# Optimization experiments

Hardware: AMD Instinct MI355X
Metric: run time of the kernel (lower is better)

## Reference

```python
import jax, jax.numpy as jnp
import numpy as np

MU = 0.34
STD = 0.04
PATCH = 32
LOG_NORM_CONST = float(np.log(STD * np.sqrt(2.0 * np.pi)))


def _patch_means(unet_output, patch):
    # unet_output: [B, C, H, W] with B == 1 (original code implicitly requires it).
    B, C, H, W = unet_output.shape
    hp, wp = H // patch, W // patch
    x = unet_output.reshape(B * C, hp, patch, wp, patch)
    # mean over batch*channel and both intra-patch axes -> [hp, wp]
    return x.mean(axis=(0, 2, 4))


def reference(unet_output, transformer_output):
    means = _patch_means(unet_output, PATCH)              # [hp, wp]
    mask = transformer_output[0] >= 0.5                   # [hp, wp]

    # Positive branch: -log(pdf(mean) + 1e-6); original uses .item() -> detached,
    # so stop_gradient reproduces the (lack of) gradient through this branch.
    m_sg = jax.lax.stop_gradient(means)
    logpdf = -0.5 * jnp.square((m_sg - MU) / STD) - LOG_NORM_CONST
    pos_term = -jnp.log(jnp.exp(logpdf) + 1e-6)

    # Negative branch: MSE against zero = mean^2 (differentiable).
    neg_term = jnp.square(means)

    maskf = mask.astype(means.dtype)
    pos_cnt = jnp.sum(maskf)
    neg_cnt = jnp.sum(1.0 - maskf)
    positive_loss = jnp.sum(pos_term * maskf) / pos_cnt
    negative_loss = jnp.sum(neg_term * (1.0 - maskf)) / neg_cnt
    return positive_loss + negative_loss


def setup_inputs() -> dict:
    key = jax.random.key(0)
    k1, k2 = jax.random.split(key)
    unet_output = jax.random.uniform(k1, (1, 1, 8192, 8192), dtype=jnp.float32)
    transformer_output = jax.random.uniform(k2, (1, 256, 256), dtype=jnp.float32)
    return {"unet_output": unet_output, "transformer_output": transformer_output}
```

## Files before the change

### kernel.cpp

```cpp
#include <hip/hip_runtime.h>
#include <math.h>

#define IMG_W 8192
#define PATCH 32
#define NPATCH 65536
#define NBLK   2048

typedef float f4 __attribute__((ext_vector_type(4)));

__global__ __launch_bounds__(256) void fused_patch_loss_kernel(
    const float* __restrict__ x, const float* __restrict__ tmask,
    float* __restrict__ p_pos, float* __restrict__ p_neg,
    float* __restrict__ p_cnt)
{
    const int wave  = threadIdx.x >> 6;
    const int lane  = threadIdx.x & 63;
    const int strip = blockIdx.x * 4 + wave;
    const int ph    = strip >> 5;
    const int seg   = strip & 31;

    const float* base = x + (size_t)ph * (PATCH * IMG_W)
                          + (size_t)seg * 256 + (size_t)lane * 4;

    float s0 = 0.0f, s1 = 0.0f, s2 = 0.0f, s3 = 0.0f;
#pragma unroll
    for (int r = 0; r < 32; r += 4) {
        const f4 v0 = __builtin_nontemporal_load(
            reinterpret_cast<const f4*>(base + (size_t)(r + 0) * IMG_W));
        const f4 v1 = __builtin_nontemporal_load(
            reinterpret_cast<const f4*>(base + (size_t)(r + 1) * IMG_W));
        const f4 v2 = __builtin_nontemporal_load(
            reinterpret_cast<const f4*>(base + (size_t)(r + 2) * IMG_W));
        const f4 v3 = __builtin_nontemporal_load(
            reinterpret_cast<const f4*>(base + (size_t)(r + 3) * IMG_W));
        s0 += (v0.x + v0.y) + (v0.z + v0.w);
        s1 += (v1.x + v1.y) + (v1.z + v1.w);
        s2 += (v2.x + v2.y) + (v2.z + v2.w);
        s3 += (v3.x + v3.y) + (v3.z + v3.w);
    }
    float s = (s0 + s1) + (s2 + s3);

    s += __shfl_down(s, 4, 64);
    s += __shfl_down(s, 2, 64);
    s += __shfl_down(s, 1, 64);

    float pos = 0.0f, neg = 0.0f, cnt = 0.0f;
    if ((lane & 7) == 0) {
        const float m = s * (1.0f / 1024.0f);
        const int patch = ph * 256 + seg * 8 + (lane >> 3);
        const float t = tmask[patch];
        const float z = (m - 0.34f) * 25.0f;
        const float logpdf = -0.5f * z * z + 2.2999373f;
        const float pterm = -logf(expf(logpdf) + 1e-6f);
        if (t >= 0.5f) { pos = pterm; cnt = 1.0f; }
        else           { neg = m * m; }
    }
    pos += __shfl_down(pos, 32, 64);
    neg += __shfl_down(neg, 32, 64);
    cnt += __shfl_down(cnt, 32, 64);
    pos += __shfl_down(pos, 16, 64);
    neg += __shfl_down(neg, 16, 64);
    cnt += __shfl_down(cnt, 16, 64);
    pos += __shfl_down(pos, 8, 64);
    neg += __shfl_down(neg, 8, 64);
    cnt += __shfl_down(cnt, 8, 64);

    __shared__ float sp[4], sn[4], sc[4];
    if (lane == 0) { sp[wave] = pos; sn[wave] = neg; sc[wave] = cnt; }
    __syncthreads();

    if (threadIdx.x == 0) {
        p_pos[blockIdx.x] = (sp[0] + sp[1]) + (sp[2] + sp[3]);
        p_neg[blockIdx.x] = (sn[0] + sn[1]) + (sn[2] + sn[3]);
        p_cnt[blockIdx.x] = (sc[0] + sc[1]) + (sc[2] + sc[3]);
    }
}

__global__ __launch_bounds__(256) void finalize_reduce_kernel(
    const float* __restrict__ p_pos, const float* __restrict__ p_neg,
    const float* __restrict__ p_cnt, float* __restrict__ out)
{
    float pos = 0.0f, neg = 0.0f, cnt = 0.0f;
#pragma unroll
    for (int i = threadIdx.x; i < NBLK; i += 256) {
        pos += p_pos[i];
        neg += p_neg[i];
        cnt += p_cnt[i];
    }

#pragma unroll
    for (int off = 32; off >= 1; off >>= 1) {
        pos += __shfl_down(pos, off, 64);
        neg += __shfl_down(neg, off, 64);
        cnt += __shfl_down(cnt, off, 64);
    }

    __shared__ float sp[4], sn[4], sc[4];
    const int wave = threadIdx.x >> 6;
    const int lane = threadIdx.x & 63;
    if (lane == 0) { sp[wave] = pos; sn[wave] = neg; sc[wave] = cnt; }
    __syncthreads();

    if (threadIdx.x == 0) {
        const float P = (sp[0] + sp[1]) + (sp[2] + sp[3]);
        const float N = (sn[0] + sn[1]) + (sn[2] + sn[3]);
        const float C = (sc[0] + sc[1]) + (sc[2] + sc[3]);
        out[0] = P / C + N / ((float)NPATCH - C);
    }
}

extern "C" void kernel_launch(void* const* d_in, const int* in_sizes, int n_in,
                              void* d_out, int out_size, void* d_ws, size_t ws_size,
                              hipStream_t stream)
{
    const float* unet  = (const float*)d_in[0];
    const float* trans = (const float*)d_in[1];
    float* out = (float*)d_out;

    float* p_pos = (float*)d_ws;
    float* p_neg = p_pos + NBLK;
    float* p_cnt = p_neg + NBLK;

    fused_patch_loss_kernel<<<NBLK, 256, 0, stream>>>(unet, trans, p_pos, p_neg, p_cnt);
    finalize_reduce_kernel<<<1, 256, 0, stream>>>(p_pos, p_neg, p_cnt, out);
}
```

Baseline: 336.2 us.

## Map one patch-row per block with row-contiguous wave loads and LDS reduction

Each block now covers a full 32-row band of patches (256 blocks of 512 threads), and each wave reads 4 full image rows contiguously instead of 32-row column strips. Per-patch sums are accumulated in 32 registers per lane, then combined across waves through a shared-memory table before the loss terms are computed. This gives fully contiguous row reads and fewer blocks, so the finalize kernel reads exactly one partial per thread. The risks are higher register pressure from 32 accumulators plus 16 vector loads in flight, and only 256 blocks on a GPU with many CUs, which may leave occupancy too low to saturate HBM bandwidth.

```diff
diff --git a/kernel.cpp b/kernel.cpp
--- a/kernel.cpp
+++ b/kernel.cpp
@@ -4,57 +4,69 @@
 #define IMG_W 8192
 #define PATCH 32
 #define NPATCH 65536
-#define NBLK   2048
+#define NBLK   256
 
 typedef float f4 __attribute__((ext_vector_type(4)));
 
-__global__ __launch_bounds__(256) void fused_patch_loss_kernel(
+__global__ __launch_bounds__(512, 2) void fused_patch_loss_kernel(
     const float* __restrict__ x, const float* __restrict__ tmask,
     float* __restrict__ p_pos, float* __restrict__ p_neg,
     float* __restrict__ p_cnt)
 {
-    const int wave  = threadIdx.x >> 6;
-    const int lane  = threadIdx.x & 63;
-    const int strip = blockIdx.x * 4 + wave;
-    const int ph    = strip >> 5;
-    const int seg   = strip & 31;
+    const int wave = threadIdx.x >> 6;
+    const int lane = threadIdx.x & 63;
+    const int ph   = blockIdx.x;
 
     const float* base = x + (size_t)ph * (PATCH * IMG_W)
-                          + (size_t)seg * 256 + (size_t)lane * 4;
+                          + (size_t)wave * (4 * IMG_W)
+                          + (size_t)lane * 4;
 
-    float s0 = 0.0f, s1 = 0.0f, s2 = 0.0f, s3 = 0.0f;
+    float acc[32];
 #pragma unroll
-    for (int r = 0; r < 32; r += 4) {
-        const f4 v0 = __builtin_nontemporal_load(
-            reinterpret_cast<const f4*>(base + (size_t)(r + 0) * IMG_W));
-        const f4 v1 = __builtin_nontemporal_load(
-            reinterpret_cast<const f4*>(base + (size_t)(r + 1) * IMG_W));
-        const f4 v2 = __builtin_nontemporal_load(
-            reinterpret_cast<const f4*>(base + (size_t)(r + 2) * IMG_W));
-        const f4 v3 = __builtin_nontemporal_load(
-            reinterpret_cast<const f4*>(base + (size_t)(r + 3) * IMG_W));
-        s0 += (v0.x + v0.y) + (v0.z + v0.w);
-        s1 += (v1.x + v1.y) + (v1.z + v1.w);
-        s2 += (v2.x + v2.y) + (v2.z + v2.w);
-        s3 += (v3.x + v3.y) + (v3.z + v3.w);
+    for (int j = 0; j < 32; ++j) acc[j] = 0.0f;
+
+#pragma unroll
+    for (int r = 0; r < 4; ++r) {
+        const float* rb = base + (size_t)r * IMG_W;
+#pragma unroll
+        for (int half = 0; half < 2; ++half) {
+            const float* hb = rb + half * (16 * 256);
+            f4 v[16];
+#pragma unroll
+            for (int i = 0; i < 16; ++i)
+                v[i] = __builtin_nontemporal_load(
+                    reinterpret_cast<const f4*>(hb + i * 256));
+#pragma unroll
+            for (int i = 0; i < 16; ++i)
+                acc[half * 16 + i] += (v[i].x + v[i].y) + (v[i].z + v[i].w);
+        }
     }
-    float s = (s0 + s1) + (s2 + s3);
 
-    s += __shfl_down(s, 4, 64);
-    s += __shfl_down(s, 2, 64);
-    s += __shfl_down(s, 1, 64);
+    __shared__ float red[8][256];
+#pragma unroll
+    for (int j = 0; j < 32; ++j) {
+        float s = acc[j];
+        s += __shfl_down(s, 4, 64);
+        s += __shfl_down(s, 2, 64);
+        s += __shfl_down(s, 1, 64);
+        if ((lane & 7) == 0) red[wave][j * 8 + (lane >> 3)] = s;
+    }
+    __syncthreads();
 
     float pos = 0.0f, neg = 0.0f, cnt = 0.0f;
-    if ((lane & 7) == 0) {
+    if (threadIdx.x < 256) {
+        const int t = threadIdx.x;
+        float s = ((red[0][t] + red[1][t]) + (red[2][t] + red[3][t]))
+                + ((red[4][t] + red[5][t]) + (red[6][t] + red[7][t]));
         const float m = s * (1.0f / 1024.0f);
-        const int patch = ph * 256 + seg * 8 + (lane >> 3);
-        const float t = tmask[patch];
+        const float tm = tmask[ph * 256 + t];
         const float z = (m - 0.34f) * 25.0f;
         const float logpdf = -0.5f * z * z + 2.2999373f;
         const float pterm = -logf(expf(logpdf) + 1e-6f);
-        if (t >= 0.5f) { pos = pterm; cnt = 1.0f; }
-        else           { neg = m * m; }
+        if (tm >= 0.5f) { pos = pterm; cnt = 1.0f; }
+        else            { neg = m * m; }
     }
+
     pos += __shfl_down(pos, 32, 64);
     neg += __shfl_down(neg, 32, 64);
     cnt += __shfl_down(cnt, 32, 64);
@@ -64,15 +76,30 @@
     pos += __shfl_down(pos, 8, 64);
     neg += __shfl_down(neg, 8, 64);
     cnt += __shfl_down(cnt, 8, 64);
+    pos += __shfl_down(pos, 4, 64);
+    neg += __shfl_down(neg, 4, 64);
+    cnt += __shfl_down(cnt, 4, 64);
+    pos += __shfl_down(pos, 2, 64);
+    neg += __shfl_down(neg, 2, 64);
+    cnt += __shfl_down(cnt, 2, 64);
+    pos += __shfl_down(pos, 1, 64);
+    neg += __shfl_down(neg, 1, 64);
+    cnt += __shfl_down(cnt, 1, 64);
 
-    __shared__ float sp[4], sn[4], sc[4];
+    __shared__ float sp[8], sn[8], sc[8];
     if (lane == 0) { sp[wave] = pos; sn[wave] = neg; sc[wave] = cnt; }
     __syncthreads();
 
     if (threadIdx.x == 0) {
-        p_pos[blockIdx.x] = (sp[0] + sp[1]) + (sp[2] + sp[3]);
-        p_neg[blockIdx.x] = (sn[0] + sn[1]) + (sn[2] + sn[3]);
-        p_cnt[blockIdx.x] = (sc[0] + sc[1]) + (sc[2] + sc[3]);
+        float P = ((sp[0] + sp[1]) + (sp[2] + sp[3]))
+                + ((sp[4] + sp[5]) + (sp[6] + sp[7]));
+        float N = ((sn[0] + sn[1]) + (sn[2] + sn[3]))
+                + ((sn[4] + sn[5]) + (sn[6] + sn[7]));
+        float C = ((sc[0] + sc[1]) + (sc[2] + sc[3]))
+                + ((sc[4] + sc[5]) + (sc[6] + sc[7]));
+        p_pos[blockIdx.x] = P;
+        p_neg[blockIdx.x] = N;
+        p_cnt[blockIdx.x] = C;
     }
 }
 
@@ -80,13 +107,10 @@
     const float* __restrict__ p_pos, const float* __restrict__ p_neg,
     const float* __restrict__ p_cnt, float* __restrict__ out)
 {
-    float pos = 0.0f, neg = 0.0f, cnt = 0.0f;
-#pragma unroll
-    for (int i = threadIdx.x; i < NBLK; i += 256) {
-        pos += p_pos[i];
-        neg += p_neg[i];
-        cnt += p_cnt[i];
-    }
+    const int t = threadIdx.x;
+    float pos = p_pos[t];
+    float neg = p_neg[t];
+    float cnt = p_cnt[t];
 
 #pragma unroll
     for (int off = 32; off >= 1; off >>= 1) {
@@ -121,6 +145,6 @@
     float* p_neg = p_pos + NBLK;
     float* p_cnt = p_neg + NBLK;
 
-    fused_patch_loss_kernel<<<NBLK, 256, 0, stream>>>(unet, trans, p_pos, p_neg, p_cnt);
+    fused_patch_loss_kernel<<<NBLK, 512, 0, stream>>>(unet, trans, p_pos, p_neg, p_cnt);
     finalize_reduce_kernel<<<1, 256, 0, stream>>>(p_pos, p_neg, p_cnt, out);
 }
```

Measured after the change: 394.7 us. 17.4% more time.

## Split patch reduction into contiguous-read partial kernel plus loss kernel

Applied to the files above, without the earlier changes.

Each wave now reads a contiguous 1 KB chunk of the image at a large stride instead of walking 32 rows of one patch strip. Every chunk's per-row partial patch sums are written to a 32x65536 intermediate buffer. A second kernel sums the 32 partials per patch, applies the loss and reduces per block, and a final kernel combines the block results. The aim is a better DRAM access pattern, paid for with an extra 8 MB intermediate write and read and one more kernel launch.

```diff
diff --git a/kernel.cpp b/kernel.cpp
--- a/kernel.cpp
+++ b/kernel.cpp
@@ -1,71 +1,83 @@
 #include <hip/hip_runtime.h>
 #include <math.h>
 
-#define IMG_W 8192
-#define PATCH 32
-#define NPATCH 65536
-#define NBLK   2048
+#define IMG_W   8192
+#define NPATCH  65536
+#define NWAVES  8192
+#define ABLK    2048
+#define BBLK    256
 
 typedef float f4 __attribute__((ext_vector_type(4)));
 
-__global__ __launch_bounds__(256) void fused_patch_loss_kernel(
-    const float* __restrict__ x, const float* __restrict__ tmask,
+__global__ __launch_bounds__(256) void patch_partial_kernel(
+    const float* __restrict__ x, float* __restrict__ inter)
+{
+    const int wave = threadIdx.x >> 6;
+    const int lane = threadIdx.x & 63;
+    const int g    = blockIdx.x * 4 + wave;
+    const int seg  = g & 31;
+    const int rho  = (g >> 5) & 31;
+    const int base = g >> 10;
+
+    const float* p0 = x + (size_t)g * 256 + (size_t)lane * 4;
+    const int k = lane >> 3;
+    float* wout = inter + (size_t)rho * NPATCH + (size_t)seg * 8 + k;
+
+#pragma unroll
+    for (int b = 0; b < 4; ++b) {
+        f4 v[8];
+#pragma unroll
+        for (int j = 0; j < 8; ++j) {
+            const int i = b * 8 + j;
+            v[j] = __builtin_nontemporal_load(
+                reinterpret_cast<const f4*>(p0 + (size_t)i * (NWAVES * 256)));
+        }
+#pragma unroll
+        for (int j = 0; j < 8; ++j) {
+            float h = (v[j].x + v[j].y) + (v[j].z + v[j].w);
+            h += __shfl_down(h, 4, 64);
+            h += __shfl_down(h, 2, 64);
+            h += __shfl_down(h, 1, 64);
+            if ((lane & 7) == 0) {
+                const int ph = base + 8 * (b * 8 + j);
+                wout[(size_t)ph * 256] = h;
+            }
+        }
+    }
+}
+
+__global__ __launch_bounds__(256) void patch_loss_kernel(
+    const float* __restrict__ inter, const float* __restrict__ tmask,
     float* __restrict__ p_pos, float* __restrict__ p_neg,
     float* __restrict__ p_cnt)
 {
-    const int wave  = threadIdx.x >> 6;
-    const int lane  = threadIdx.x & 63;
-    const int strip = blockIdx.x * 4 + wave;
-    const int ph    = strip >> 5;
-    const int seg   = strip & 31;
+    const int p = blockIdx.x * 256 + threadIdx.x;
 
-    const float* base = x + (size_t)ph * (PATCH * IMG_W)
-                          + (size_t)seg * 256 + (size_t)lane * 4;
+    float s = 0.0f;
+#pragma unroll
+    for (int rho = 0; rho < 32; ++rho)
+        s += inter[(size_t)rho * NPATCH + p];
 
-    float s0 = 0.0f, s1 = 0.0f, s2 = 0.0f, s3 = 0.0f;
-#pragma unroll
-    for (int r = 0; r < 32; r += 4) {
-        const f4 v0 = __builtin_nontemporal_load(
-            reinterpret_cast<const f4*>(base + (size_t)(r + 0) * IMG_W));
-        const f4 v1 = __builtin_nontemporal_load(
-            reinterpret_cast<const f4*>(base + (size_t)(r + 1) * IMG_W));
-        const f4 v2 = __builtin_nontemporal_load(
-            reinterpret_cast<const f4*>(base + (size_t)(r + 2) * IMG_W));
-        const f4 v3 = __builtin_nontemporal_load(
-            reinterpret_cast<const f4*>(base + (size_t)(r + 3) * IMG_W));
-        s0 += (v0.x + v0.y) + (v0.z + v0.w);
-        s1 += (v1.x + v1.y) + (v1.z + v1.w);
-        s2 += (v2.x + v2.y) + (v2.z + v2.w);
-        s3 += (v3.x + v3.y) + (v3.z + v3.w);
-    }
-    float s = (s0 + s1) + (s2 + s3);
-
-    s += __shfl_down(s, 4, 64);
-    s += __shfl_down(s, 2, 64);
-    s += __shfl_down(s, 1, 64);
+    const float m = s * (1.0f / 1024.0f);
+    const float tm = tmask[p];
+    const float z = (m - 0.34f) * 25.0f;
+    const float logpdf = -0.5f * z * z + 2.2999373f;
+    const float pterm = -logf(expf(logpdf) + 1e-6f);
 
     float pos = 0.0f, neg = 0.0f, cnt = 0.0f;
-    if ((lane & 7) == 0) {
-        const float m = s * (1.0f / 1024.0f);
-        const int patch = ph * 256 + seg * 8 + (lane >> 3);
-        const float t = tmask[patch];
-        const float z = (m - 0.34f) * 25.0f;
-        const float logpdf = -0.5f * z * z + 2.2999373f;
-        const float pterm = -logf(expf(logpdf) + 1e-6f);
-        if (t >= 0.5f) { pos = pterm; cnt = 1.0f; }
-        else           { neg = m * m; }
+    if (tm >= 0.5f) { pos = pterm; cnt = 1.0f; }
+    else            { neg = m * m; }
+
+#pragma unroll
+    for (int off = 32; off >= 1; off >>= 1) {
+        pos += __shfl_down(pos, off, 64);
+        neg += __shfl_down(neg, off, 64);
+        cnt += __shfl_down(cnt, off, 64);
     }
-    pos += __shfl_down(pos, 32, 64);
-    neg += __shfl_down(neg, 32, 64);
-    cnt += __shfl_down(cnt, 32, 64);
-    pos += __shfl_down(pos, 16, 64);
-    neg += __shfl_down(neg, 16, 64);
-    cnt += __shfl_down(cnt, 16, 64);
-    pos += __shfl_down(pos, 8, 64);
-    neg += __shfl_down(neg, 8, 64);
-    cnt += __shfl_down(cnt, 8, 64);
 
     __shared__ float sp[4], sn[4], sc[4];
+    const int wave = threadIdx.x >> 6;
+    const int lane = threadIdx.x & 63;
     if (lane == 0) { sp[wave] = pos; sn[wave] = neg; sc[wave] = cnt; }
     __syncthreads();
 
@@ -80,13 +92,10 @@
     const float* __restrict__ p_pos, const float* __restrict__ p_neg,
     const float* __restrict__ p_cnt, float* __restrict__ out)
 {
-    float pos = 0.0f, neg = 0.0f, cnt = 0.0f;
-#pragma unroll
-    for (int i = threadIdx.x; i < NBLK; i += 256) {
-        pos += p_pos[i];
-        neg += p_neg[i];
-        cnt += p_cnt[i];
-    }
+    const int t = threadIdx.x;
+    float pos = p_pos[t];
+    float neg = p_neg[t];
+    float cnt = p_cnt[t];
 
 #pragma unroll
     for (int off = 32; off >= 1; off >>= 1) {
@@ -117,10 +126,12 @@
     const float* trans = (const float*)d_in[1];
     float* out = (float*)d_out;
 
-    float* p_pos = (float*)d_ws;
-    float* p_neg = p_pos + NBLK;
-    float* p_cnt = p_neg + NBLK;
+    float* inter = (float*)d_ws;
+    float* p_pos = inter + 32 * NPATCH;
+    float* p_neg = p_pos + BBLK;
+    float* p_cnt = p_neg + BBLK;
 
-    fused_patch_loss_kernel<<<NBLK, 256, 0, stream>>>(unet, trans, p_pos, p_neg, p_cnt);
+    patch_partial_kernel<<<ABLK, 256, 0, stream>>>(unet, inter);
+    patch_loss_kernel<<<BBLK, 256, 0, stream>>>(inter, trans, p_pos, p_neg, p_cnt);
     finalize_reduce_kernel<<<1, 256, 0, stream>>>(p_pos, p_neg, p_cnt, out);
 }
```

Result: slower. 349.5 us (+4.0%).
